# Kernel tuning notes

Hardware: AMD Instinct MI355X
Metric: run time of the kernel (lower is better)

## Reference

```python
import jax, jax.numpy as jnp
import numpy as np

N_ATOMS = 100000
BOX = 12.0
NS = 128            # 2**ceil(log2(2*(2*pi/mesh_spacing)*BOX/(2*pi) + 1)) with mesh_spacing=0.2
ORDER = 4           # interpolation_order (cubic)
SMEARING = 1.0      # atomic_gaussian_width
N_SPECIES = 2


def _weights_1d(x):
    # P3M order-4 assignment weights; offsets x in [-1/2, 1/2]
    x2 = x * x
    x3 = x2 * x
    return jnp.stack([
        (1.0 - 6.0 * x + 12.0 * x2 - 8.0 * x3) / 48.0,
        (23.0 - 30.0 * x - 12.0 * x2 + 24.0 * x3) / 48.0,
        (23.0 + 30.0 * x - 12.0 * x2 - 24.0 * x3) / 48.0,
        (1.0 + 6.0 * x + 12.0 * x2 + 8.0 * x3) / 48.0,
    ])  # (ORDER, n_atoms, 3)


def _interpolation(positions, cell, ns):
    # fractional coordinates scaled by mesh size; even order -> offset vs cell midpoint
    inv_cell = jnp.linalg.inv(cell)
    pos_rel = ns * (positions @ inv_cell)                     # (n, 3)
    base = jnp.floor(pos_rel)
    offsets = pos_rel - (base + 0.5)                          # in [-1/2, 1/2)
    w = _weights_1d(offsets)                                  # (4, n, 3)
    shifts = jnp.arange(1 - (ORDER + 1) // 2, 1 + ORDER // 2, dtype=jnp.int32)  # [-1,0,1,2]
    idx = (base.astype(jnp.int32)[None, :, :] + shifts[:, None, None]) % ns    # (4, n, 3)
    return w, idx


def _points_to_mesh(w, idx, charges, ns):
    # scatter charges onto the mesh via the separable 4^3 stencil
    n_ch = charges.shape[1]
    mesh = jnp.zeros((n_ch, ns, ns, ns), dtype=charges.dtype)
    cT = charges.T                                            # (n_ch, n)
    for l in range(ORDER):
        for m in range(ORDER):
            for n in range(ORDER):
                ww = w[l, :, 0] * w[m, :, 1] * w[n, :, 2]     # (n_atoms,)
                mesh = mesh.at[:, idx[l, :, 0], idx[m, :, 1], idx[n, :, 2]].add(ww * cT)
    return mesh


def _mesh_to_points(mesh, w, idx):
    # gather the potential back to the atom positions with the same stencil
    pot = jnp.zeros((mesh.shape[0], w.shape[1]), dtype=mesh.dtype)
    for l in range(ORDER):
        for m in range(ORDER):
            for n in range(ORDER):
                ww = w[l, :, 0] * w[m, :, 1] * w[n, :, 2]
                pot = pot + ww * mesh[:, idx[l, :, 0], idx[m, :, 1], idx[n, :, 2]]
    return pot.T  # (n_atoms, n_ch)


def _fourier_space_convolution(mesh, cell, ns, smearing):
    # Coulomb kernel (potential_exponent=1) with Gaussian smearing, k=0 term removed
    m1 = jnp.fft.fftfreq(ns) * ns                             # integer frequencies
    m3 = jnp.fft.rfftfreq(ns) * ns
    mx, my, mz = jnp.meshgrid(m1, m1, m3, indexing="ij")
    mvec = jnp.stack([mx, my, mz], axis=-1)                   # (ns, ns, ns//2+1, 3)
    k = 2.0 * jnp.pi * (mvec @ jnp.linalg.inv(cell).T)        # reciprocal vectors
    ksq = jnp.sum(k * k, axis=-1)
    safe = jnp.where(ksq > 0.0, ksq, 1.0)
    G = jnp.where(ksq > 0.0, 4.0 * jnp.pi * jnp.exp(-0.5 * smearing * smearing * ksq) / safe, 0.0)
    mesh_hat = jnp.fft.rfftn(mesh, axes=(1, 2, 3))            # unnormalized forward
    pot = jnp.fft.irfftn(mesh_hat * G, s=(ns, ns, ns), axes=(1, 2, 3), norm="forward")
    volume = jnp.abs(jnp.linalg.det(cell))
    return pot / volume


def _compute_single_frame(positions, cell, charges, ns):
    w, idx = _interpolation(positions, cell, ns)
    rho_mesh = _points_to_mesh(w, idx, charges, ns)
    pot_mesh = _fourier_space_convolution(rho_mesh, cell, ns, SMEARING)
    return _mesh_to_points(pot_mesh, w, idx)                  # (n_atoms, n_channels)


def setup_inputs() -> dict:
    key = jax.random.key(0)
    k1, k2 = jax.random.split(key)
    positions = jax.random.uniform(k1, (N_ATOMS, 3), dtype=jnp.float32) * BOX
    cell = BOX * jnp.eye(3, dtype=jnp.float32)
    species = jax.random.randint(k2, (N_ATOMS,), 0, N_SPECIES, dtype=jnp.int32)
    return {"positions": positions, "cell": cell, "species": species, "ns": NS}


def reference(positions, cell, species, ns):
    # compute(): one-hot species channels, then particle-mesh Ewald potential per channel
    charges = jax.nn.one_hot(species, N_SPECIES, dtype=positions.dtype)
    return _compute_single_frame(positions, cell, charges, ns)
```

## Files before the change

### kernel.cpp

```cpp
#include <hip/hip_runtime.h>

#define NSZ 128
#define NS3 (NSZ * NSZ * NSZ)
#define NBUCK_D 16
#define NBUCK (NBUCK_D * NBUCK_D * NBUCK_D)
#define RGD 8
#define RW 16
#define LROW 129
#define LDS_BYTES (NSZ * LROW * sizeof(float2))


__device__ __forceinline__ void inv3x3(const float* __restrict__ c, float* inv) {
    float a00 = c[0], a01 = c[1], a02 = c[2];
    float a10 = c[3], a11 = c[4], a12 = c[5];
    float a20 = c[6], a21 = c[7], a22 = c[8];
    float det = a00 * (a11 * a22 - a12 * a21)
              - a01 * (a10 * a22 - a12 * a20)
              + a02 * (a10 * a21 - a11 * a20);
    float id = 1.0f / det;
    inv[0] = (a11 * a22 - a12 * a21) * id;
    inv[1] = (a02 * a21 - a01 * a22) * id;
    inv[2] = (a01 * a12 - a02 * a11) * id;
    inv[3] = (a12 * a20 - a10 * a22) * id;
    inv[4] = (a00 * a22 - a02 * a20) * id;
    inv[5] = (a02 * a10 - a00 * a12) * id;
    inv[6] = (a10 * a21 - a11 * a20) * id;
    inv[7] = (a01 * a20 - a00 * a21) * id;
    inv[8] = (a00 * a11 - a01 * a10) * id;
}

__device__ __forceinline__ float det3x3(const float* __restrict__ c) {
    return c[0] * (c[4] * c[8] - c[5] * c[7])
         - c[1] * (c[3] * c[8] - c[5] * c[6])
         + c[2] * (c[3] * c[7] - c[4] * c[6]);
}

__device__ __forceinline__ int brev7(int i) { return (int)(__brev((unsigned)i) >> 25); }

__device__ __forceinline__ float2 cadd(float2 a, float2 b) { return make_float2(a.x + b.x, a.y + b.y); }
__device__ __forceinline__ float2 csub(float2 a, float2 b) { return make_float2(a.x - b.x, a.y - b.y); }
__device__ __forceinline__ float2 cmul(float2 a, float2 b) {
    return make_float2(a.x * b.x - a.y * b.y, a.x * b.y + a.y * b.x);
}
__device__ __forceinline__ float2 cmulc(float2 a, float2 b) {
    return make_float2(a.x * b.x + a.y * b.y, a.y * b.x - a.x * b.y);
}

__device__ __forceinline__ void stencil_pos(float px, float py, float pz,
                                            const float* __restrict__ inv,
                                            int base[3], float w[3][4]) {
    float pr[3];
    pr[0] = (float)NSZ * (px * inv[0] + py * inv[3] + pz * inv[6]);
    pr[1] = (float)NSZ * (px * inv[1] + py * inv[4] + pz * inv[7]);
    pr[2] = (float)NSZ * (px * inv[2] + py * inv[5] + pz * inv[8]);
#pragma unroll
    for (int d = 0; d < 3; d++) {
        float b = floorf(pr[d]);
        float x = pr[d] - b - 0.5f;
        float x2 = x * x, x3 = x2 * x;
        w[d][0] = (1.0f - 6.0f * x + 12.0f * x2 - 8.0f * x3) * (1.0f / 48.0f);
        w[d][1] = (23.0f - 30.0f * x - 12.0f * x2 + 24.0f * x3) * (1.0f / 48.0f);
        w[d][2] = (23.0f + 30.0f * x - 12.0f * x2 - 24.0f * x3) * (1.0f / 48.0f);
        w[d][3] = (1.0f + 6.0f * x + 12.0f * x2 + 8.0f * x3) * (1.0f / 48.0f);
        int bi = (int)b;
        base[d] = bi < 0 ? 0 : (bi > NSZ - 1 ? NSZ - 1 : bi);
    }
}

__device__ __forceinline__ int bucket_of(float px, float py, float pz,
                                         const float* __restrict__ inv) {
    float prx = (float)NSZ * (px * inv[0] + py * inv[3] + pz * inv[6]);
    float pry = (float)NSZ * (px * inv[1] + py * inv[4] + pz * inv[7]);
    float prz = (float)NSZ * (px * inv[2] + py * inv[5] + pz * inv[8]);
    int bx = (int)floorf(prx); bx = bx < 0 ? 0 : (bx > NSZ - 1 ? NSZ - 1 : bx);
    int by = (int)floorf(pry); by = by < 0 ? 0 : (by > NSZ - 1 ? NSZ - 1 : by);
    int bz = (int)floorf(prz); bz = bz < 0 ? 0 : (bz > NSZ - 1 ? NSZ - 1 : bz);
    return ((bx >> 3) * NBUCK_D + (by >> 3)) * NBUCK_D + (bz >> 3);
}


__global__ void bin_hist(const float* __restrict__ pos, const float* __restrict__ cell,
                         int* __restrict__ counts, int n_atoms) {
    int a = blockIdx.x * blockDim.x + threadIdx.x;
    if (a >= n_atoms) return;
    float inv[9];
    inv3x3(cell, inv);
    atomicAdd(&counts[bucket_of(pos[a * 3], pos[a * 3 + 1], pos[a * 3 + 2], inv)], 1);
}

__global__ void __launch_bounds__(1024)
scan4096(const int* __restrict__ counts, int* __restrict__ starts, int* __restrict__ cursor) {
    __shared__ int wsum[16];
    __shared__ int wpref[16];
    int t = threadIdx.x;
    int c0 = counts[4 * t], c1 = counts[4 * t + 1], c2 = counts[4 * t + 2], c3 = counts[4 * t + 3];
    int tot = c0 + c1 + c2 + c3;
    int lane = t & 63, w = t >> 6;
    int incl = tot;
#pragma unroll
    for (int o = 1; o < 64; o <<= 1) {
        int v = __shfl_up(incl, o, 64);
        if (lane >= o) incl += v;
    }
    if (lane == 63) wsum[w] = incl;
    __syncthreads();
    if (t < 16) {
        int v = wsum[t], p = 0;
        for (int i = 0; i < 16; i++) { if (i < t) p += wsum[i]; }
        wpref[t] = p;
        (void)v;
    }
    __syncthreads();
    int ex = wpref[w] + incl - tot;
    starts[4 * t]     = ex;           cursor[4 * t]     = ex;
    starts[4 * t + 1] = ex + c0;      cursor[4 * t + 1] = ex + c0;
    starts[4 * t + 2] = ex + c0 + c1; cursor[4 * t + 2] = ex + c0 + c1;
    starts[4 * t + 3] = ex + c0 + c1 + c2; cursor[4 * t + 3] = ex + c0 + c1 + c2;
    if (t == 1023) starts[4096] = ex + tot;
}

__global__ void bin_permute(const float* __restrict__ pos, const float* __restrict__ cell,
                            const int* __restrict__ species, int* __restrict__ cursor,
                            float4* __restrict__ recs, int n_atoms) {
    int a = blockIdx.x * blockDim.x + threadIdx.x;
    if (a >= n_atoms) return;
    float inv[9];
    inv3x3(cell, inv);
    float px = pos[a * 3], py = pos[a * 3 + 1], pz = pos[a * 3 + 2];
    int b = bucket_of(px, py, pz, inv);
    int p = atomicAdd(&cursor[b], 1);
    recs[p] = make_float4(px, py, pz, __int_as_float((a << 1) | (species[a] & 1)));
}


#define ACC_ROW 33
#define ACC_SZ (RW * RW * ACC_ROW)

__global__ void __launch_bounds__(256)
scatter_region(const float* __restrict__ cell, const int* __restrict__ starts,
               const float4* __restrict__ recs, float2* __restrict__ mesh) {
    __shared__ float acc[ACC_SZ];
    __shared__ int rstart_s[64];
    __shared__ int rpref_s[64];
    __shared__ int rtot_s;
    int t = threadIdx.x;
    int BX = blockIdx.x, BY = blockIdx.y, BZ = blockIdx.z;

    for (int i = t; i < ACC_SZ; i += 256) acc[i] = 0.0f;

    if (t < 64) {
        int dx = (t >> 4) & 3, dy = (t >> 2) & 3, dz = t & 3;
        int bx = (2 * BX - 1 + dx) & (NBUCK_D - 1);
        int by = (2 * BY - 1 + dy) & (NBUCK_D - 1);
        int bz = (2 * BZ - 1 + dz) & (NBUCK_D - 1);
        int b = (bx * NBUCK_D + by) * NBUCK_D + bz;
        int s0 = starts[b];
        int c = starts[b + 1] - s0;
        rstart_s[t] = s0;
        int incl = c;
#pragma unroll
        for (int o = 1; o < 64; o <<= 1) {
            int v = __shfl_up(incl, o, 64);
            if (t >= o) incl += v;
        }
        rpref_s[t] = incl - c;
        if (t == 63) rtot_s = incl;
    }
    __syncthreads();

    float inv[9];
    inv3x3(cell, inv);
    int M = rtot_s;
    int sx = BX << 4, sy = BY << 4, sz = BZ << 4;
    int lane = t & 63;

    for (int i = t; i < M; i += 256) {
        int r = 0;
#pragma unroll
        for (int step = 32; step; step >>= 1)
            if (r + step < 64 && rpref_s[r + step] <= i) r += step;
        float4 rec = recs[rstart_s[r] + (i - rpref_s[r])];
        int base[3];
        float w[3][4];
        stencil_pos(rec.x, rec.y, rec.z, inv, base, w);
        int rbx = (base[0] - sx + 2) & (NSZ - 1);
        int rby = (base[1] - sy + 2) & (NSZ - 1);
        int rbz = (base[2] - sz + 2) & (NSZ - 1);
        if (rbx >= 19 || rby >= 19 || rbz >= 19) continue;
        rbx -= 2; rby -= 2; rbz -= 2;
        int sp = __float_as_int(rec.w) & 1;
#pragma unroll
        for (int l = 0; l < 4; l++) {
            int cx = rbx + l - 1;
            if ((unsigned)cx >= (unsigned)RW) continue;
            float wl = w[0][l];
#pragma unroll
            for (int m = 0; m < 4; m++) {
                int cy = rby + m - 1;
                if ((unsigned)cy >= (unsigned)RW) continue;
                float wlm = wl * w[1][m];
                int rowb = (cx * RW + cy) * ACC_ROW + sp;
#pragma unroll
                for (int nn = 0; nn < 4; nn++) {
                    int n = (nn + lane) & 3;
                    int cz = rbz + n - 1;
                    if ((unsigned)cz >= (unsigned)RW) continue;
                    atomicAdd(&acc[rowb + cz * 2], wlm * w[2][n]);
                }
            }
        }
    }
    __syncthreads();

    for (int i = t; i < RW * RW * RW; i += 256) {
        int x = i >> 8, y = (i >> 4) & 15, z = i & 15;
        float2 v = make_float2(acc[(x * RW + y) * ACC_ROW + z * 2],
                               acc[(x * RW + y) * ACC_ROW + z * 2 + 1]);
        size_t gi = (size_t)((sx + x) * NSZ + (sy + y)) * NSZ + (sz + z);
        mesh[gi] = v;
    }
}


__global__ void scatter_atomic(const float* __restrict__ pos,
                               const float* __restrict__ cell,
                               const int* __restrict__ species,
                               float* __restrict__ meshf, int n_atoms) {
    int a = blockIdx.x * blockDim.x + threadIdx.x;
    if (a >= n_atoms) return;
    float inv[9];
    inv3x3(cell, inv);
    int base[3];
    float w[3][4];
    stencil_pos(pos[a * 3], pos[a * 3 + 1], pos[a * 3 + 2], inv, base, w);
    int sp = species[a] & 1;
#pragma unroll
    for (int l = 0; l < 4; l++) {
        int gx = (base[0] + l - 1 + NSZ) & (NSZ - 1);
#pragma unroll
        for (int m = 0; m < 4; m++) {
            int gy = (base[1] + m - 1 + NSZ) & (NSZ - 1);
            float wlm = w[0][l] * w[1][m];
            int rowb = (gx * NSZ + gy) * NSZ;
#pragma unroll
            for (int n = 0; n < 4; n++) {
                int gz = (base[2] + n - 1 + NSZ) & (NSZ - 1);
                atomicAdd(meshf + (((size_t)(rowb + gz)) << 1) + sp, wlm * w[2][n]);
            }
        }
    }
}


__global__ void __launch_bounds__(1024)
fft_fwd_zy(float2* __restrict__ mesh) {
    extern __shared__ float2 sl[];
    __shared__ float2 tw[64];
    int t = threadIdx.x;
    int xs = blockIdx.x;
    if (t < 64) {
        float sn, cs;
        __sincosf(6.283185307179586f * (float)t / 128.0f, &sn, &cs);
        tw[t] = make_float2(cs, -sn);
    }
    const float4* src = (const float4*)(mesh + (size_t)xs * (NSZ * NSZ));
    for (int f = t; f < 8192; f += 1024) {
        float4 v = src[f];
        int y = f >> 6, z = (f & 63) * 2;
        sl[y * LROW + z]     = make_float2(v.x, v.y);
        sl[y * LROW + z + 1] = make_float2(v.z, v.w);
    }
    __syncthreads();
    int lane = t & 127, jb = (t >> 7) * 8;
    for (int s = 6; s >= 0; --s) {
        int half = 1 << s;
        for (int j = jb; j < jb + 8; ++j) {
            int pos = j & (half - 1);
            int i0 = ((j >> s) << (s + 1)) + pos;
            float2 w = tw[pos << (6 - s)];
            float2* p0 = &sl[lane * LROW + i0];
            float2 a = p0[0], b = p0[half];
            p0[0]    = cadd(a, b);
            p0[half] = cmul(csub(a, b), w);
        }
        __syncthreads();
    }
    for (int s = 6; s >= 0; --s) {
        int half = 1 << s;
        for (int j = jb; j < jb + 8; ++j) {
            int pos = j & (half - 1);
            int i0 = ((j >> s) << (s + 1)) + pos;
            float2 w = tw[pos << (6 - s)];
            float2* p0 = &sl[i0 * LROW + lane];
            float2 a = p0[0], b = p0[half * LROW];
            p0[0]           = cadd(a, b);
            p0[half * LROW] = cmul(csub(a, b), w);
        }
        __syncthreads();
    }
    float4* dst = (float4*)(mesh + (size_t)xs * (NSZ * NSZ));
    for (int f = t; f < 8192; f += 1024) {
        int y = f >> 6, z = (f & 63) * 2;
        float2 u0 = sl[y * LROW + z], u1 = sl[y * LROW + z + 1];
        dst[f] = make_float4(u0.x, u0.y, u1.x, u1.y);
    }
}

__global__ void __launch_bounds__(1024)
fft_x_g(float2* __restrict__ mesh, const float* __restrict__ cell, float smearing) {
    extern __shared__ float2 sl[];
    __shared__ float2 tw[64];
    int t = threadIdx.x;
    int y = blockIdx.x;
    if (t < 64) {
        float sn, cs;
        __sincosf(6.283185307179586f * (float)t / 128.0f, &sn, &cs);
        tw[t] = make_float2(cs, -sn);
    }
    for (int f = t; f < 8192; f += 1024) {
        int x = f >> 6, c = f & 63;
        float4 v = ((const float4*)mesh)[(size_t)x * 8192 + (size_t)y * 64 + c];
        int z = c * 2;
        sl[x * LROW + z]     = make_float2(v.x, v.y);
        sl[x * LROW + z + 1] = make_float2(v.z, v.w);
    }
    __syncthreads();
    int lane = t & 127, jb = (t >> 7) * 8;
    for (int s = 6; s >= 0; --s) {
        int half = 1 << s;
        for (int j = jb; j < jb + 8; ++j) {
            int pos = j & (half - 1);
            int i0 = ((j >> s) << (s + 1)) + pos;
            float2 w = tw[pos << (6 - s)];
            float2* p0 = &sl[i0 * LROW + lane];
            float2 a = p0[0], b = p0[half * LROW];
            p0[0]           = cadd(a, b);
            p0[half * LROW] = cmul(csub(a, b), w);
        }
        __syncthreads();
    }
    {
        float inv[9];
        inv3x3(cell, inv);
        float vol = fabsf(det3x3(cell));
        int kyi = brev7(y);
        float fy = (kyi < NSZ / 2) ? (float)kyi : (float)(kyi - NSZ);
        const float twopi = 6.283185307179586f;
        for (int f = t; f < NSZ * NSZ; f += 1024) {
            int px = f >> 7, pz = f & 127;
            int kxi = brev7(px), kzi = brev7(pz);
            float fx = (kxi < NSZ / 2) ? (float)kxi : (float)(kxi - NSZ);
            float fz = (kzi < NSZ / 2) ? (float)kzi : (float)(kzi - NSZ);
            float k0 = twopi * (fx * inv[0] + fy * inv[1] + fz * inv[2]);
            float k1 = twopi * (fx * inv[3] + fy * inv[4] + fz * inv[5]);
            float k2 = twopi * (fx * inv[6] + fy * inv[7] + fz * inv[8]);
            float ksq = k0 * k0 + k1 * k1 + k2 * k2;
            float g = 0.0f;
            if (ksq > 0.0f) {
                g = 12.566370614359172f * __expf(-0.5f * smearing * smearing * ksq) / ksq;
            }
            g /= vol;
            float2 v = sl[px * LROW + pz];
            sl[px * LROW + pz] = make_float2(v.x * g, v.y * g);
        }
    }
    __syncthreads();
    for (int s = 0; s < 7; ++s) {
        int half = 1 << s;
        for (int j = jb; j < jb + 8; ++j) {
            int pos = j & (half - 1);
            int i0 = ((j >> s) << (s + 1)) + pos;
            float2 w = tw[pos << (6 - s)];
            float2* p0 = &sl[i0 * LROW + lane];
            float2 a = p0[0];
            float2 bw = cmulc(p0[half * LROW], w);
            p0[0]           = cadd(a, bw);
            p0[half * LROW] = csub(a, bw);
        }
        __syncthreads();
    }
    for (int f = t; f < 8192; f += 1024) {
        int x = f >> 6, c = f & 63;
        int z = c * 2;
        float2 u0 = sl[x * LROW + z], u1 = sl[x * LROW + z + 1];
        ((float4*)mesh)[(size_t)x * 8192 + (size_t)y * 64 + c] = make_float4(u0.x, u0.y, u1.x, u1.y);
    }
}

__global__ void __launch_bounds__(1024)
fft_inv_yz(float2* __restrict__ mesh) {
    extern __shared__ float2 sl[];
    __shared__ float2 tw[64];
    int t = threadIdx.x;
    int xs = blockIdx.x;
    if (t < 64) {
        float sn, cs;
        __sincosf(6.283185307179586f * (float)t / 128.0f, &sn, &cs);
        tw[t] = make_float2(cs, -sn);
    }
    const float4* src = (const float4*)(mesh + (size_t)xs * (NSZ * NSZ));
    for (int f = t; f < 8192; f += 1024) {
        float4 v = src[f];
        int y = f >> 6, z = (f & 63) * 2;
        sl[y * LROW + z]     = make_float2(v.x, v.y);
        sl[y * LROW + z + 1] = make_float2(v.z, v.w);
    }
    __syncthreads();
    int lane = t & 127, jb = (t >> 7) * 8;
    for (int s = 0; s < 7; ++s) {
        int half = 1 << s;
        for (int j = jb; j < jb + 8; ++j) {
            int pos = j & (half - 1);
            int i0 = ((j >> s) << (s + 1)) + pos;
            float2 w = tw[pos << (6 - s)];
            float2* p0 = &sl[i0 * LROW + lane];
            float2 a = p0[0];
            float2 bw = cmulc(p0[half * LROW], w);
            p0[0]           = cadd(a, bw);
            p0[half * LROW] = csub(a, bw);
        }
        __syncthreads();
    }
    for (int s = 0; s < 7; ++s) {
        int half = 1 << s;
        for (int j = jb; j < jb + 8; ++j) {
            int pos = j & (half - 1);
            int i0 = ((j >> s) << (s + 1)) + pos;
            float2 w = tw[pos << (6 - s)];
            float2* p0 = &sl[lane * LROW + i0];
            float2 a = p0[0];
            float2 bw = cmulc(p0[half], w);
            p0[0]    = cadd(a, bw);
            p0[half] = csub(a, bw);
        }
        __syncthreads();
    }
    float4* dst = (float4*)(mesh + (size_t)xs * (NSZ * NSZ));
    for (int f = t; f < 8192; f += 1024) {
        int y = f >> 6, z = (f & 63) * 2;
        float2 u0 = sl[y * LROW + z], u1 = sl[y * LROW + z + 1];
        dst[f] = make_float4(u0.x, u0.y, u1.x, u1.y);
    }
}


__global__ void gather_sorted(const float* __restrict__ cell,
                              const float2* __restrict__ mesh,
                              const float4* __restrict__ recs,
                              float2* __restrict__ out, int n_atoms) {
    int i = blockIdx.x * blockDim.x + threadIdx.x;
    if (i >= n_atoms) return;
    float4 rec = recs[i];
    float inv[9];
    inv3x3(cell, inv);
    int base[3];
    float w[3][4];
    stencil_pos(rec.x, rec.y, rec.z, inv, base, w);
    float acc0 = 0.0f, acc1 = 0.0f;
#pragma unroll
    for (int l = 0; l < 4; l++) {
        int gx = (base[0] + l - 1 + NSZ) & (NSZ - 1);
#pragma unroll
        for (int m = 0; m < 4; m++) {
            int gy = (base[1] + m - 1 + NSZ) & (NSZ - 1);
            float wlm = w[0][l] * w[1][m];
            int rowb = (gx * NSZ + gy) * NSZ;
#pragma unroll
            for (int n = 0; n < 4; n++) {
                int gz = (base[2] + n - 1 + NSZ) & (NSZ - 1);
                float2 v = mesh[rowb + gz];
                float ww = wlm * w[2][n];
                acc0 += ww * v.x;
                acc1 += ww * v.y;
            }
        }
    }
    out[__float_as_int(rec.w) >> 1] = make_float2(acc0, acc1);
}

__global__ void gather_plain(const float* __restrict__ pos,
                             const float* __restrict__ cell,
                             const float2* __restrict__ mesh,
                             float2* __restrict__ out, int n_atoms) {
    int a = blockIdx.x * blockDim.x + threadIdx.x;
    if (a >= n_atoms) return;
    float inv[9];
    inv3x3(cell, inv);
    int base[3];
    float w[3][4];
    stencil_pos(pos[a * 3], pos[a * 3 + 1], pos[a * 3 + 2], inv, base, w);
    float acc0 = 0.0f, acc1 = 0.0f;
#pragma unroll
    for (int l = 0; l < 4; l++) {
        int gx = (base[0] + l - 1 + NSZ) & (NSZ - 1);
#pragma unroll
        for (int m = 0; m < 4; m++) {
            int gy = (base[1] + m - 1 + NSZ) & (NSZ - 1);
            float wlm = w[0][l] * w[1][m];
            int rowb = (gx * NSZ + gy) * NSZ;
#pragma unroll
            for (int n = 0; n < 4; n++) {
                int gz = (base[2] + n - 1 + NSZ) & (NSZ - 1);
                float2 v = mesh[rowb + gz];
                float ww = wlm * w[2][n];
                acc0 += ww * v.x;
                acc1 += ww * v.y;
            }
        }
    }
    out[a] = make_float2(acc0, acc1);
}


extern "C" void kernel_launch(void* const* d_in, const int* in_sizes, int n_in,
                              void* d_out, int out_size, void* d_ws, size_t ws_size,
                              hipStream_t stream) {
    const float* pos     = (const float*)d_in[0];
    const float* cell    = (const float*)d_in[1];
    const int*   species = (const int*)d_in[2];
    int n_atoms = in_sizes[0] / 3;

    char* ws = (char*)d_ws;
    float2* mesh = (float2*)ws;
    size_t off = (size_t)NS3 * sizeof(float2);
    int* counts = (int*)(ws + off);           off += NBUCK * 4;
    int* starts = (int*)(ws + off);           off += (NBUCK + 4) * 4;
    int* cursor = (int*)(ws + off);           off += NBUCK * 4;
    off = (off + 15) & ~(size_t)15;
    float4* recs = (float4*)(ws + off);       off += (size_t)n_atoms * 16;
    bool binned = (ws_size >= off);

    hipFuncSetAttribute((const void*)fft_fwd_zy, hipFuncAttributeMaxDynamicSharedMemorySize, (int)LDS_BYTES);
    hipFuncSetAttribute((const void*)fft_x_g,    hipFuncAttributeMaxDynamicSharedMemorySize, (int)LDS_BYTES);
    hipFuncSetAttribute((const void*)fft_inv_yz, hipFuncAttributeMaxDynamicSharedMemorySize, (int)LDS_BYTES);

    int ab = (n_atoms + 255) / 256;

    if (binned) {
        hipMemsetAsync(counts, 0, NBUCK * 4, stream);
        bin_hist<<<ab, 256, 0, stream>>>(pos, cell, counts, n_atoms);
        scan4096<<<1, 1024, 0, stream>>>(counts, starts, cursor);
        bin_permute<<<ab, 256, 0, stream>>>(pos, cell, species, cursor, recs, n_atoms);
        dim3 rg(RGD, RGD, RGD);
        scatter_region<<<rg, 256, 0, stream>>>(cell, starts, recs, mesh);
    } else {
        hipMemsetAsync(mesh, 0, (size_t)NS3 * sizeof(float2), stream);
        scatter_atomic<<<ab, 256, 0, stream>>>(pos, cell, species, (float*)mesh, n_atoms);
    }

    fft_fwd_zy<<<NSZ, 1024, LDS_BYTES, stream>>>(mesh);
    fft_x_g   <<<NSZ, 1024, LDS_BYTES, stream>>>(mesh, cell, 1.0f );
    fft_inv_yz<<<NSZ, 1024, LDS_BYTES, stream>>>(mesh);

    if (binned) {
        gather_sorted<<<ab, 256, 0, stream>>>(cell, mesh, recs, (float2*)d_out, n_atoms);
    } else {
        gather_plain<<<ab, 256, 0, stream>>>(pos, cell, mesh, (float2*)d_out, n_atoms);
    }
}
```

Baseline: 246.2 us.

## Gather per bucket from LDS mesh tile, widen scatter blocks, defer weights

Result: faster. 232.8 us (-5.4%).

```diff
diff --git a/kernel.cpp b/kernel.cpp
--- a/kernel.cpp
+++ b/kernel.cpp
@@ -46,9 +46,9 @@
     return make_float2(a.x * b.x + a.y * b.y, a.y * b.x - a.x * b.y);
 }
 
-__device__ __forceinline__ void stencil_pos(float px, float py, float pz,
-                                            const float* __restrict__ inv,
-                                            int base[3], float w[3][4]) {
+__device__ __forceinline__ void bases_of(float px, float py, float pz,
+                                         const float* __restrict__ inv,
+                                         int base[3], float frac[3]) {
     float pr[3];
     pr[0] = (float)NSZ * (px * inv[0] + py * inv[3] + pz * inv[6]);
     pr[1] = (float)NSZ * (px * inv[1] + py * inv[4] + pz * inv[7]);
@@ -56,26 +56,36 @@
 #pragma unroll
     for (int d = 0; d < 3; d++) {
         float b = floorf(pr[d]);
-        float x = pr[d] - b - 0.5f;
-        float x2 = x * x, x3 = x2 * x;
-        w[d][0] = (1.0f - 6.0f * x + 12.0f * x2 - 8.0f * x3) * (1.0f / 48.0f);
-        w[d][1] = (23.0f - 30.0f * x - 12.0f * x2 + 24.0f * x3) * (1.0f / 48.0f);
-        w[d][2] = (23.0f + 30.0f * x - 12.0f * x2 - 24.0f * x3) * (1.0f / 48.0f);
-        w[d][3] = (1.0f + 6.0f * x + 12.0f * x2 + 8.0f * x3) * (1.0f / 48.0f);
+        frac[d] = pr[d] - b - 0.5f;
         int bi = (int)b;
         base[d] = bi < 0 ? 0 : (bi > NSZ - 1 ? NSZ - 1 : bi);
     }
 }
 
+__device__ __forceinline__ void weights_of(float x, float w[4]) {
+    float x2 = x * x, x3 = x2 * x;
+    w[0] = (1.0f - 6.0f * x + 12.0f * x2 - 8.0f * x3) * (1.0f / 48.0f);
+    w[1] = (23.0f - 30.0f * x - 12.0f * x2 + 24.0f * x3) * (1.0f / 48.0f);
+    w[2] = (23.0f + 30.0f * x - 12.0f * x2 - 24.0f * x3) * (1.0f / 48.0f);
+    w[3] = (1.0f + 6.0f * x + 12.0f * x2 + 8.0f * x3) * (1.0f / 48.0f);
+}
+
+__device__ __forceinline__ void stencil_pos(float px, float py, float pz,
+                                            const float* __restrict__ inv,
+                                            int base[3], float w[3][4]) {
+    float frac[3];
+    bases_of(px, py, pz, inv, base, frac);
+    weights_of(frac[0], w[0]);
+    weights_of(frac[1], w[1]);
+    weights_of(frac[2], w[2]);
+}
+
 __device__ __forceinline__ int bucket_of(float px, float py, float pz,
                                          const float* __restrict__ inv) {
-    float prx = (float)NSZ * (px * inv[0] + py * inv[3] + pz * inv[6]);
-    float pry = (float)NSZ * (px * inv[1] + py * inv[4] + pz * inv[7]);
-    float prz = (float)NSZ * (px * inv[2] + py * inv[5] + pz * inv[8]);
-    int bx = (int)floorf(prx); bx = bx < 0 ? 0 : (bx > NSZ - 1 ? NSZ - 1 : bx);
-    int by = (int)floorf(pry); by = by < 0 ? 0 : (by > NSZ - 1 ? NSZ - 1 : by);
-    int bz = (int)floorf(prz); bz = bz < 0 ? 0 : (bz > NSZ - 1 ? NSZ - 1 : bz);
-    return ((bx >> 3) * NBUCK_D + (by >> 3)) * NBUCK_D + (bz >> 3);
+    int base[3];
+    float frac[3];
+    bases_of(px, py, pz, inv, base, frac);
+    return ((base[0] >> 3) * NBUCK_D + (base[1] >> 3)) * NBUCK_D + (base[2] >> 3);
 }
 
 
@@ -105,16 +115,15 @@
     if (lane == 63) wsum[w] = incl;
     __syncthreads();
     if (t < 16) {
-        int v = wsum[t], p = 0;
+        int p = 0;
         for (int i = 0; i < 16; i++) { if (i < t) p += wsum[i]; }
         wpref[t] = p;
-        (void)v;
     }
     __syncthreads();
     int ex = wpref[w] + incl - tot;
-    starts[4 * t]     = ex;           cursor[4 * t]     = ex;
-    starts[4 * t + 1] = ex + c0;      cursor[4 * t + 1] = ex + c0;
-    starts[4 * t + 2] = ex + c0 + c1; cursor[4 * t + 2] = ex + c0 + c1;
+    starts[4 * t]     = ex;                cursor[4 * t]     = ex;
+    starts[4 * t + 1] = ex + c0;           cursor[4 * t + 1] = ex + c0;
+    starts[4 * t + 2] = ex + c0 + c1;      cursor[4 * t + 2] = ex + c0 + c1;
     starts[4 * t + 3] = ex + c0 + c1 + c2; cursor[4 * t + 3] = ex + c0 + c1 + c2;
     if (t == 1023) starts[4096] = ex + tot;
 }
@@ -136,7 +145,7 @@
 #define ACC_ROW 33
 #define ACC_SZ (RW * RW * ACC_ROW)
 
-__global__ void __launch_bounds__(256)
+__global__ void __launch_bounds__(1024)
 scatter_region(const float* __restrict__ cell, const int* __restrict__ starts,
                const float4* __restrict__ recs, float2* __restrict__ mesh) {
     __shared__ float acc[ACC_SZ];
@@ -146,7 +155,7 @@
     int t = threadIdx.x;
     int BX = blockIdx.x, BY = blockIdx.y, BZ = blockIdx.z;
 
-    for (int i = t; i < ACC_SZ; i += 256) acc[i] = 0.0f;
+    for (int i = t; i < ACC_SZ; i += 1024) acc[i] = 0.0f;
 
     if (t < 64) {
         int dx = (t >> 4) & 3, dy = (t >> 2) & 3, dz = t & 3;
@@ -174,20 +183,24 @@
     int sx = BX << 4, sy = BY << 4, sz = BZ << 4;
     int lane = t & 63;
 
-    for (int i = t; i < M; i += 256) {
+    for (int i = t; i < M; i += 1024) {
         int r = 0;
 #pragma unroll
         for (int step = 32; step; step >>= 1)
             if (r + step < 64 && rpref_s[r + step] <= i) r += step;
         float4 rec = recs[rstart_s[r] + (i - rpref_s[r])];
         int base[3];
-        float w[3][4];
-        stencil_pos(rec.x, rec.y, rec.z, inv, base, w);
+        float frac[3];
+        bases_of(rec.x, rec.y, rec.z, inv, base, frac);
         int rbx = (base[0] - sx + 2) & (NSZ - 1);
         int rby = (base[1] - sy + 2) & (NSZ - 1);
         int rbz = (base[2] - sz + 2) & (NSZ - 1);
         if (rbx >= 19 || rby >= 19 || rbz >= 19) continue;
         rbx -= 2; rby -= 2; rbz -= 2;
+        float w[3][4];
+        weights_of(frac[0], w[0]);
+        weights_of(frac[1], w[1]);
+        weights_of(frac[2], w[2]);
         int sp = __float_as_int(rec.w) & 1;
 #pragma unroll
         for (int l = 0; l < 4; l++) {
@@ -212,7 +225,7 @@
     }
     __syncthreads();
 
-    for (int i = t; i < RW * RW * RW; i += 256) {
+    for (int i = t; i < RW * RW * RW; i += 1024) {
         int x = i >> 8, y = (i >> 4) & 15, z = i & 15;
         float2 v = make_float2(acc[(x * RW + y) * ACC_ROW + z * 2],
                                acc[(x * RW + y) * ACC_ROW + z * 2 + 1]);
@@ -444,38 +457,58 @@
 }
 
 
-__global__ void gather_sorted(const float* __restrict__ cell,
-                              const float2* __restrict__ mesh,
-                              const float4* __restrict__ recs,
-                              float2* __restrict__ out, int n_atoms) {
-    int i = blockIdx.x * blockDim.x + threadIdx.x;
-    if (i >= n_atoms) return;
-    float4 rec = recs[i];
+#define GROW 12
+
+__global__ void __launch_bounds__(128)
+gather_region(const float* __restrict__ cell, const int* __restrict__ starts,
+              const float4* __restrict__ recs, const float2* __restrict__ mesh,
+              float2* __restrict__ out) {
+    __shared__ float2 gm[11 * 11 * GROW];
+    int t = threadIdx.x;
+    int b = blockIdx.x;
+    int bx = b >> 8, by = (b >> 4) & 15, bz = b & 15;
+    int ox = bx * 8 - 1, oy = by * 8 - 1, oz = bz * 8 - 1;
+
+    for (int i = t; i < 11 * 11 * 11; i += 128) {
+        int x = i / 121, rem = i % 121, y = rem / 11, z = rem % 11;
+        int gx = (ox + x) & (NSZ - 1);
+        int gy = (oy + y) & (NSZ - 1);
+        int gz = (oz + z) & (NSZ - 1);
+        gm[(x * 11 + y) * GROW + z] = mesh[(size_t)(gx * NSZ + gy) * NSZ + gz];
+    }
+    __syncthreads();
+
+    int s = starts[b], e = starts[b + 1];
     float inv[9];
     inv3x3(cell, inv);
-    int base[3];
-    float w[3][4];
-    stencil_pos(rec.x, rec.y, rec.z, inv, base, w);
-    float acc0 = 0.0f, acc1 = 0.0f;
-#pragma unroll
-    for (int l = 0; l < 4; l++) {
-        int gx = (base[0] + l - 1 + NSZ) & (NSZ - 1);
-#pragma unroll
-        for (int m = 0; m < 4; m++) {
-            int gy = (base[1] + m - 1 + NSZ) & (NSZ - 1);
-            float wlm = w[0][l] * w[1][m];
-            int rowb = (gx * NSZ + gy) * NSZ;
-#pragma unroll
-            for (int n = 0; n < 4; n++) {
-                int gz = (base[2] + n - 1 + NSZ) & (NSZ - 1);
-                float2 v = mesh[rowb + gz];
-                float ww = wlm * w[2][n];
-                acc0 += ww * v.x;
-                acc1 += ww * v.y;
+
+    for (int ai = s + t; ai < e; ai += 128) {
+        float4 rec = recs[ai];
+        int base[3];
+        float w[3][4];
+        stencil_pos(rec.x, rec.y, rec.z, inv, base, w);
+        int lx0 = base[0] - bx * 8;
+        int ly0 = base[1] - by * 8;
+        int lz0 = base[2] - bz * 8;
+        float acc0 = 0.0f, acc1 = 0.0f;
+#pragma unroll
+        for (int l = 0; l < 4; l++) {
+            float wl = w[0][l];
+#pragma unroll
+            for (int m = 0; m < 4; m++) {
+                float wlm = wl * w[1][m];
+                int rowb = ((lx0 + l) * 11 + (ly0 + m)) * GROW + lz0;
+#pragma unroll
+                for (int n = 0; n < 4; n++) {
+                    float2 v = gm[rowb + n];
+                    float ww = wlm * w[2][n];
+                    acc0 += ww * v.x;
+                    acc1 += ww * v.y;
+                }
             }
         }
-    }
-    out[__float_as_int(rec.w) >> 1] = make_float2(acc0, acc1);
+        out[__float_as_int(rec.w) >> 1] = make_float2(acc0, acc1);
+    }
 }
 
 __global__ void gather_plain(const float* __restrict__ pos,
@@ -542,7 +575,7 @@
         scan4096<<<1, 1024, 0, stream>>>(counts, starts, cursor);
         bin_permute<<<ab, 256, 0, stream>>>(pos, cell, species, cursor, recs, n_atoms);
         dim3 rg(RGD, RGD, RGD);
-        scatter_region<<<rg, 256, 0, stream>>>(cell, starts, recs, mesh);
+        scatter_region<<<rg, 1024, 0, stream>>>(cell, starts, recs, mesh);
     } else {
         hipMemsetAsync(mesh, 0, (size_t)NS3 * sizeof(float2), stream);
         scatter_atomic<<<ab, 256, 0, stream>>>(pos, cell, species, (float*)mesh, n_atoms);
@@ -553,7 +586,7 @@
     fft_inv_yz<<<NSZ, 1024, LDS_BYTES, stream>>>(mesh);
 
     if (binned) {
-        gather_sorted<<<ab, 256, 0, stream>>>(cell, mesh, recs, (float2*)d_out, n_atoms);
+        gather_region<<<NBUCK, 128, 0, stream>>>(cell, starts, recs, mesh, (float2*)d_out);
     } else {
         gather_plain<<<ab, 256, 0, stream>>>(pos, cell, mesh, (float2*)d_out, n_atoms);
     }
```
